# Optimization experiments

Hardware: AMD Instinct MI355X
Metric: run time of the kernel (lower is better)

The kernel has to match this reference:

```python
import jax, jax.numpy as jnp
import numpy as np

N, D, E, P, L = 50000, 128, 800000, 9, 3
EPS = 1e-5  # torch nn.LayerNorm default eps


def _layernorm(x, g, b):
    m = jnp.mean(x, axis=-1, keepdims=True)
    v = jnp.mean((x - m) ** 2, axis=-1, keepdims=True)
    return (x - m) * jax.lax.rsqrt(v + EPS) * g + b


def _pol_transform(x, M, onehot):
    # x: (N,d), M: (P,d,d), onehot: (N,P). Equivalent to bmm(x[n] @ M[pol[n]])
    # without materializing the (N,d,d) gathered map tensor.
    return jnp.einsum('nd,np,pdk->nk', x, onehot, M)


def setup_inputs() -> dict:
    key = jax.random.key(0)
    ks = jax.random.split(key, 12)
    s = 1.0 / np.sqrt(D)  # xavier-ish scale
    f32 = jnp.float32
    return {
        'x': jax.random.normal(ks[0], (N, D), f32),
        'edge_index': jax.random.randint(ks[1], (2, E), 0, N),
        'ring_polarities': jax.random.randint(ks[2], (N,), 0, P),
        'Wr': jax.random.normal(ks[3], (L, D, D), f32) * s,          # restriction weights
        'S': jax.random.normal(ks[4], (L, P, D, D), f32) * s,        # send_maps
        'dS': jax.random.normal(ks[5], (L, P, D, D), f32) * 0.01,    # delta_send
        'R': jax.random.normal(ks[6], (L, P, D, D), f32) * s,        # receive_maps
        'dR': jax.random.normal(ks[7], (L, P, D, D), f32) * 0.01,    # delta_receive
        'res_scale': jnp.full((L,), 0.92, f32),
        'W1': jax.random.normal(ks[8], (L, D, D), f32) * s,          # update Linear 1
        'b1': jnp.zeros((L, D), f32),
        'ln_g': jnp.ones((L, D), f32),                               # update LayerNorm
        'ln_b': jnp.zeros((L, D), f32),
        'W2': jax.random.normal(ks[9], (L, D, D), f32) * s,          # update Linear 2
        'b2': jnp.zeros((L, D), f32),
        'norm_g': jnp.ones((L, D), f32),                             # output LayerNorm
        'norm_b': jnp.zeros((L, D), f32),
    }


def reference(x, edge_index, ring_polarities, Wr, S, dS, R, dR, res_scale,
              W1, b1, ln_g, ln_b, W2, b2, norm_g, norm_b):
    src, tgt = edge_index[0], edge_index[1]
    pol = ring_polarities % P
    onehot = jax.nn.one_hot(pol, P, dtype=x.dtype)  # (N,P)
    # deg is accumulated over row(=src) in the original code, then used to
    # normalize the scatter over col(=tgt) -- preserved faithfully.
    deg = jax.ops.segment_sum(jnp.ones((E,), x.dtype), src, num_segments=N)
    deg_norm = (1.0 / jnp.clip(deg, 1.0))[:, None]  # (N,1)

    residual = x
    for l in range(L):
        # send transform: map depends only on src-node polarity, so apply
        # per-node then gather (algebraically identical to per-edge bmm).
        xt = _pol_transform(x, S[l] + dS[l], onehot)          # (N,D)
        msg = xt[src] @ Wr[l].T                               # (E,D) restriction per edge
        agg = jax.ops.segment_sum(msg, tgt, num_segments=N)   # index_add scatter
        # receive transform depends only on tgt polarity; linear, so it
        # commutes with the sum over incoming edges.
        out = _pol_transform(agg, R[l] + dR[l], onehot) * deg_norm
        # update MLP (dropout inactive in eval)
        h = jax.nn.relu(_layernorm(out @ W1[l].T + b1[l], ln_g[l], ln_b[l]))
        out = h @ W2[l].T + b2[l]
        out = res_scale[l] * out + x                           # in==out residual
        x = _layernorm(out, norm_g[l], norm_b[l])
    return x + residual  # stack-level residual (res_proj is None, dims match)
```

## Files before the change

kernel.cpp:

```cpp
#include <hip/hip_runtime.h>
#include <hip/hip_bf16.h>

constexpr int N_ = 50000;
constexpr int D_ = 128;
constexpr int E_ = 800000;
constexpr int P_ = 9;
constexpr int L_ = 3;
constexpr float EPS_ = 1e-5f;

constexpr int TM = 128;
constexpr int CHUNK = 4096;
constexpr int NBK = (E_ + CHUNK - 1) / CHUNK;
constexpr int NBUK = 196;
constexpr int HHALF = 256 * NBK;
constexpr int HTOT = 2 * HHALF;
constexpr int NSB = HTOT / 1024;
constexpr int MAT = L_ * P_;

typedef short bf16x8 __attribute__((ext_vector_type(8)));
typedef float f32x4 __attribute__((ext_vector_type(4)));

#define GLD16(gp, lp)                                                        \
    __builtin_amdgcn_global_load_lds(                                        \
        (const __attribute__((address_space(1))) unsigned int*)(gp),         \
        (__attribute__((address_space(3))) unsigned int*)(lp), 16, 0, 0)

__device__ inline unsigned short f2bf(float f) {
    __hip_bfloat16 h = __float2bfloat16(f);
    return *reinterpret_cast<unsigned short*>(&h);
}
__device__ inline float bflo(unsigned u) { return __uint_as_float(u << 16); }
__device__ inline float bfhi(unsigned u) { return __uint_as_float(u & 0xffff0000u); }
__device__ inline float bf2f(unsigned short h) {
    return __uint_as_float((unsigned)h << 16);
}
__device__ inline unsigned pack2bf(float a, float b) {
    return (unsigned)f2bf(a) | ((unsigned)f2bf(b) << 16);
}


__global__ __launch_bounds__(256) void setup_nk(const int* __restrict__ ring,
                                                int* __restrict__ pol,
                                                int* __restrict__ bcnt,
                                                const int* __restrict__ ei,
                                                int* __restrict__ histG) {
    __shared__ int h[P_];
    __shared__ int hT[256], hS[256];
    int blk = blockIdx.x, tid = threadIdx.x;
    if (tid < P_) h[tid] = 0;
    hT[tid] = 0;
    hS[tid] = 0;
    __syncthreads();
    int n = blk * 256 + tid;
    if (n < N_) {
        int p = ring[n] % P_;
        pol[n] = p;
        atomicAdd(&h[p], 1);
    }
    int base = blk * CHUNK;
#pragma unroll
    for (int i = 0; i < CHUNK / 256; ++i) {
        int e = base + tid + i * 256;
        if (e < E_) {
            atomicAdd(&hS[ei[e] >> 8], 1);
            atomicAdd(&hT[ei[E_ + e] >> 8], 1);
        }
    }
    __syncthreads();
    if (tid < P_ && h[tid] > 0) atomicAdd(&bcnt[tid], h[tid]);
    histG[tid * NBK + blk] = hT[tid];
    histG[HHALF + tid * NBK + blk] = hS[tid];
}


__global__ __launch_bounds__(1024) void scanH1(int* __restrict__ a,
                                               int* __restrict__ blkSum) {
    __shared__ int wsum[16];
    int tid = threadIdx.x, lane = tid & 63, wid = tid >> 6;
    int idx = blockIdx.x * 1024 + tid;
    int v = a[idx];
    int inc = v;
#pragma unroll
    for (int o = 1; o < 64; o <<= 1) {
        int t = __shfl_up(inc, o, 64);
        if (lane >= o) inc += t;
    }
    if (lane == 63) wsum[wid] = inc;
    __syncthreads();
    if (tid < 16) {
        int s = wsum[tid];
#pragma unroll
        for (int o = 1; o < 16; o <<= 1) {
            int t = __shfl_up(s, o, 64);
            if (tid >= o) s += t;
        }
        wsum[tid] = s;
    }
    __syncthreads();
    int wexcl = (wid == 0) ? 0 : wsum[wid - 1];
    a[idx] = wexcl + inc - v;
    if (tid == 1023) blkSum[blockIdx.x] = wsum[15];
}

__global__ void scanH2(const int* __restrict__ blkSum, int* __restrict__ blkOff,
                       int* __restrict__ offT, const int* __restrict__ bcnt,
                       int* __restrict__ boff, int* __restrict__ tileOff) {
    if (threadIdx.x != 0) return;
    int run = 0;
    for (int i = 0; i < NSB; ++i) {
        blkOff[i] = run;
        run += blkSum[i];
    }
    offT[N_] = E_;
    boff[0] = 0;
    tileOff[0] = 0;
    for (int p = 0; p < P_; ++p) {
        boff[p + 1] = boff[p] + bcnt[p];
        tileOff[p + 1] = tileOff[p] + (bcnt[p] + TM - 1) / TM;
    }
}

__global__ __launch_bounds__(1024) void scanH3(int* __restrict__ a,
                                               const int* __restrict__ blkOff) {
    int idx = blockIdx.x * 1024 + threadIdx.x;
    a[idx] += blkOff[blockIdx.x];
}


__global__ __launch_bounds__(256) void scatterTS(const int* __restrict__ ei,
                                                 const int* __restrict__ histG,
                                                 unsigned* __restrict__ bufT,
                                                 unsigned char* __restrict__ bufS8) {
    __shared__ int ldsT[256], ldsS[256];
    int blk = blockIdx.x, tid = threadIdx.x;
    ldsT[tid] = histG[tid * NBK + blk];
    ldsS[tid] = histG[HHALF + tid * NBK + blk] - E_;
    __syncthreads();
    int base = blk * CHUNK;
#pragma unroll
    for (int i = 0; i < CHUNK / 256; ++i) {
        int e = base + tid + i * 256;
        if (e < E_) {
            int s = ei[e], t = ei[E_ + e];
            int pT = atomicAdd(&ldsT[t >> 8], 1);
            bufT[pT] = ((unsigned)t << 16) | (unsigned)s;
            int pS = atomicAdd(&ldsS[s >> 8], 1);
            bufS8[pS] = (unsigned char)(s & 255);
        }
    }
}


__global__ __launch_bounds__(256) void finalize3(
    const unsigned* __restrict__ bufT, const unsigned char* __restrict__ bufS8,
    const int* __restrict__ histG, int* __restrict__ offT,
    unsigned short* __restrict__ eSrc, float* __restrict__ dnorm,
    const int* __restrict__ pol, const int* __restrict__ boff,
    int* __restrict__ bcur, int* __restrict__ blist) {
    __shared__ int s0[256];
    __shared__ int s1[256];
    int bb = blockIdx.x, tid = threadIdx.x;

    if (bb < NBUK) {
        int b = bb;
        int start = histG[b * NBK];
        int end = histG[(b + 1) * NBK];
        s0[tid] = 0;
        __syncthreads();
        for (int i = start + tid; i < end; i += 256)
            atomicAdd(&s0[(bufT[i] >> 16) & 255], 1);
        __syncthreads();
        if (tid < 64) {
            int b0 = 4 * tid;
            int v0 = s0[b0], v1 = s0[b0 + 1], v2 = s0[b0 + 2], v3 = s0[b0 + 3];
            int lsum = v0 + v1 + v2 + v3;
            int inc = lsum;
#pragma unroll
            for (int o = 1; o < 64; o <<= 1) {
                int t = __shfl_up(inc, o, 64);
                if (tid >= o) inc += t;
            }
            int excl = inc - lsum;
            s1[b0] = excl;
            s1[b0 + 1] = excl + v0;
            s1[b0 + 2] = excl + v0 + v1;
            s1[b0 + 3] = excl + v0 + v1 + v2;
        }
        __syncthreads();
        int node = (b << 8) + tid;
        if (node < N_) offT[node] = start + s1[tid];
        __syncthreads();
        for (int i = start + tid; i < end; i += 256) {
            unsigned pk = bufT[i];
            int pos = start + atomicAdd(&s1[(pk >> 16) & 255], 1);
            eSrc[pos] = (unsigned short)(pk & 0xFFFF);
        }
    } else if (bb < 2 * NBUK) {
        int b = bb - NBUK;
        int start = histG[HHALF + b * NBK] - E_;
        int end = histG[HHALF + (b + 1) * NBK] - E_;
        s0[tid] = 0;
        __syncthreads();
        for (int i = start + tid; i < end; i += 256) atomicAdd(&s0[bufS8[i]], 1);
        __syncthreads();
        int node = (b << 8) + tid;
        if (node < N_) {
            int dg = s0[tid];
            dnorm[node] = 1.f / (float)(dg > 1 ? dg : 1);
        }
    } else {
        int b = bb - 2 * NBUK;
        if (tid < P_) s0[tid] = 0;
        __syncthreads();
        int n = b * 256 + tid;
        int p = 0, loc = 0;
        bool act = (n < N_);
        if (act) {
            p = pol[n];
            loc = atomicAdd(&s0[p], 1);
        }
        __syncthreads();
        if (tid < P_ && s0[tid] > 0) s1[tid] = atomicAdd(&bcur[tid], s0[tid]);
        __syncthreads();
        if (act) blist[boff[p] + s1[p] + loc] = n;
    }
}


constexpr int GCONV = N_ * D_ / 4 / 256;
constexpr int GS = L_ * P_ * D_ * D_ / 256;
constexpr int GW2 = L_ * D_ * D_ / 256;
constexpr int GSPL = (MAT + 6) * 16384 / 256;
constexpr int GPREP = GCONV + 1 + GS + GW2 + GSPL;

__global__ __launch_bounds__(256) void prep_all(
    const float* __restrict__ x, unsigned short* __restrict__ xb,
    unsigned short* __restrict__ bufAb, unsigned short* __restrict__ bufBb,
    const float* __restrict__ S, const float* __restrict__ dS,
    unsigned short* __restrict__ Sb,
    const float* __restrict__ W2, unsigned short* __restrict__ W2b,
    const float* __restrict__ R, const float* __restrict__ dR,
    const float* __restrict__ W1, const float* __restrict__ Wr,
    unsigned short* __restrict__ Arh, unsigned short* __restrict__ Arl,
    unsigned short* __restrict__ W1h, unsigned short* __restrict__ W1l,
    unsigned short* __restrict__ Wrth, unsigned short* __restrict__ Wrtl) {
    int b = blockIdx.x, tid = threadIdx.x;
    if (b < GCONV) {
        int i = b * 256 + tid;
        float4 v = ((const float4*)x)[i];
        ushort4 o;
        o.x = f2bf(v.x); o.y = f2bf(v.y); o.z = f2bf(v.z); o.w = f2bf(v.w);
        ((ushort4*)xb)[i] = o;
    } else if (b < GCONV + 1) {
        if (tid < 64) {
            ((unsigned*)(xb + (size_t)N_ * D_))[tid] = 0;
            ((unsigned*)(bufAb + (size_t)N_ * D_))[tid] = 0;
            ((unsigned*)(bufBb + (size_t)N_ * D_))[tid] = 0;
        }
    } else if (b < GCONV + 1 + GS) {
        int idx = (b - GCONV - 1) * 256 + tid;
        int base = idx / (D_ * D_);
        int rem = idx % (D_ * D_);
        int c = rem / D_, d = rem % D_;
        size_t in = (size_t)base * D_ * D_ + (size_t)d * D_ + c;
        Sb[idx] = f2bf(S[in] + dS[in]);
    } else if (b < GCONV + 1 + GS + GW2) {
        int idx = (b - GCONV - 1 - GS) * 256 + tid;
        W2b[idx] = f2bf(W2[idx]);
    } else {
        constexpr int SZ1 = MAT * 16384;
        constexpr int SZ2 = SZ1 + 3 * 16384;
        int idx = (b - GCONV - 1 - GS - GW2) * 256 + tid;
        float v;
        unsigned short* oh;
        unsigned short* ol;
        int j;
        if (idx < SZ1) {
            v = R[idx] + dR[idx];
            oh = Arh; ol = Arl; j = idx;
        } else if (idx < SZ2) {
            j = idx - SZ1;
            v = W1[j];
            oh = W1h; ol = W1l;
        } else {
            j = idx - SZ2;
            int l = j >> 14, rem = j & 16383;
            int d = rem >> 7, i = rem & 127;
            v = Wr[(l << 14) + i * 128 + d];
            oh = Wrth; ol = Wrtl;
        }
        unsigned short h = f2bf(v);
        oh[j] = h;
        ol[j] = f2bf(v - bf2f(h));
    }
}


template <bool APM, bool BPM, bool OUT_SPLIT>
__global__ __launch_bounds__(256) void small_mfma(
    const unsigned short* __restrict__ Ah, const unsigned short* __restrict__ Al,
    const unsigned short* __restrict__ Bh, const unsigned short* __restrict__ Bl,
    unsigned short* __restrict__ Oh, unsigned short* __restrict__ Ol) {
    __shared__ unsigned short stg[(OUT_SPLIT ? 2 : 1) * 64 * 136];
    int tid = threadIdx.x, b = blockIdx.x;
    int mat = b >> 1, rb = b & 1;
    int l = mat / P_;
    size_t aoff = (size_t)(APM ? mat : l) * 16384 + (size_t)rb * 8192;
    size_t boff = (size_t)(BPM ? mat : l) * 16384;
    const unsigned short* ahp = Ah + aoff;
    const unsigned short* alp = Al + aoff;
    const unsigned short* bhp = Bh + boff;
    const unsigned short* blp = Bl + boff;

    int lane = tid & 63, wave = tid >> 6;
    int n = lane & 15, q = lane >> 4;
    int wr = wave * 16;

    f32x4 acc[8];
#pragma unroll
    for (int t = 0; t < 8; ++t) acc[t] = (f32x4){0.f, 0.f, 0.f, 0.f};

    int arow = (wr + n) * 128;
#pragma unroll
    for (int kc = 0; kc < 4; ++kc) {
        int ko = kc * 32 + q * 8;
        bf16x8 avh = *(const bf16x8*)(ahp + arow + ko);
        bf16x8 avl = *(const bf16x8*)(alp + arow + ko);
#pragma unroll
        for (int t = 0; t < 8; ++t) {
            int brow = (t * 16 + n) * 128;
            bf16x8 bvh = *(const bf16x8*)(bhp + brow + ko);
            bf16x8 bvl = *(const bf16x8*)(blp + brow + ko);
            acc[t] = __builtin_amdgcn_mfma_f32_16x16x32_bf16(avh, bvh, acc[t], 0, 0, 0);
            acc[t] = __builtin_amdgcn_mfma_f32_16x16x32_bf16(avh, bvl, acc[t], 0, 0, 0);
            acc[t] = __builtin_amdgcn_mfma_f32_16x16x32_bf16(avl, bvh, acc[t], 0, 0, 0);
        }
    }
#pragma unroll
    for (int t = 0; t < 8; ++t)
#pragma unroll
        for (int r = 0; r < 4; ++r) {
            int row = wr + q * 4 + r;
            float v = acc[t][r];
            unsigned short h = f2bf(v);
            stg[row * 136 + t * 16 + n] = h;
            if constexpr (OUT_SPLIT)
                stg[64 * 136 + row * 136 + t * 16 + n] = f2bf(v - bf2f(h));
        }
    __syncthreads();
    size_t obase = (size_t)mat * 16384 + (size_t)rb * 8192;
#pragma unroll
    for (int i = 0; i < 4; ++i) {
        int c = tid + i * 256;
        int r = c >> 4, off = c & 15;
        *(uint4*)(Oh + obase + r * 128 + off * 8) =
            *(const uint4*)(stg + r * 136 + off * 8);
        if constexpr (OUT_SPLIT)
            *(uint4*)(Ol + obase + r * 128 + off * 8) =
                *(const uint4*)(stg + 64 * 136 + r * 136 + off * 8);
    }
}


__device__ inline void accum_row(float* acc, uint4 r) {
    acc[0] += bflo(r.x); acc[1] += bfhi(r.x);
    acc[2] += bflo(r.y); acc[3] += bfhi(r.y);
    acc[4] += bflo(r.z); acc[5] += bfhi(r.z);
    acc[6] += bflo(r.w); acc[7] += bfhi(r.w);
}

__global__ __launch_bounds__(256) void aggregate_bf(const unsigned short* __restrict__ xt,
                                                    const int* __restrict__ offT,
                                                    const unsigned short* __restrict__ eSrc,
                                                    unsigned short* __restrict__ agg) {
    int nd = blockIdx.x * 4 + (threadIdx.x >> 6);
    if (nd >= N_) return;
    int l = threadIdx.x & 63;
    int g = l >> 4, c16 = l & 15;
    int beg = offT[nd], end = offT[nd + 1];

    float acc[8];
#pragma unroll
    for (int k = 0; k < 8; ++k) acc[k] = 0.f;

    for (int base = beg; base < end; base += 64) {
        int cnt = min(64, end - base);
        int idxv = (l < cnt) ? (int)eSrc[base + l] : 0;
        int steps = (cnt + 3) >> 2;
        int j = 0;
        for (; j + 3 < steps; j += 4) {
            int e0 = 4 * j + g, e1 = e0 + 4, e2 = e0 + 8, e3 = e0 + 12;
            int i0 = __shfl(idxv, e0, 64);
            int i1 = __shfl(idxv, e1, 64);
            int i2 = __shfl(idxv, e2, 64);
            int i3 = __shfl(idxv, e3, 64);
            int r0 = (e0 < cnt) ? i0 : N_;
            int r1 = (e1 < cnt) ? i1 : N_;
            int r2 = (e2 < cnt) ? i2 : N_;
            int r3 = (e3 < cnt) ? i3 : N_;
            uint4 v0 = ((const uint4*)(xt + (size_t)r0 * D_))[c16];
            uint4 v1 = ((const uint4*)(xt + (size_t)r1 * D_))[c16];
            uint4 v2 = ((const uint4*)(xt + (size_t)r2 * D_))[c16];
            uint4 v3 = ((const uint4*)(xt + (size_t)r3 * D_))[c16];
            accum_row(acc, v0);
            accum_row(acc, v1);
            accum_row(acc, v2);
            accum_row(acc, v3);
        }
        for (; j < steps; ++j) {
            int e0 = 4 * j + g;
            int i0 = __shfl(idxv, e0, 64);
            int r0 = (e0 < cnt) ? i0 : N_;
            uint4 v0 = ((const uint4*)(xt + (size_t)r0 * D_))[c16];
            accum_row(acc, v0);
        }
    }
#pragma unroll
    for (int k = 0; k < 8; ++k) {
        acc[k] += __shfl_xor(acc[k], 16, 64);
        acc[k] += __shfl_xor(acc[k], 32, 64);
    }
    if (g == 0) {
        uint4 o;
        o.x = (unsigned)f2bf(acc[0]) | ((unsigned)f2bf(acc[1]) << 16);
        o.y = (unsigned)f2bf(acc[2]) | ((unsigned)f2bf(acc[3]) << 16);
        o.z = (unsigned)f2bf(acc[4]) | ((unsigned)f2bf(acc[5]) << 16);
        o.w = (unsigned)f2bf(acc[6]) | ((unsigned)f2bf(acc[7]) << 16);
        ((uint4*)(agg + (size_t)nd * D_))[c16] = o;
    }
}


__device__ inline void stage_B_async(const unsigned short* __restrict__ B,
                                     unsigned short* sB, int wave, int lane) {
    int rsub = lane >> 4, cl = lane & 15;
#pragma unroll
    for (int j = 0; j < 4; ++j) {
        int seg = wave * 4 + j;
        int row = seg * 4 + rsub;
        GLD16(B + row * 128 + ((cl ^ (row & 15)) << 3), sB + seg * 512);
    }
}

#define XCH_FRAG(dst, Pl, Ph, kc)                                            \
    {                                                                        \
        unsigned a0 = __shfl(Pl[2 * (kc)], s0, 64);                          \
        unsigned b0 = __shfl(Pl[2 * (kc) + 1], s0, 64);                      \
        unsigned a1 = __shfl(Ph[2 * (kc)], s0, 64);                          \
        unsigned b1 = __shfl(Ph[2 * (kc) + 1], s0, 64);                      \
        unsigned a2 = __shfl(Pl[2 * (kc)], s1, 64);                          \
        unsigned b2 = __shfl(Pl[2 * (kc) + 1], s1, 64);                      \
        unsigned a3 = __shfl(Ph[2 * (kc)], s1, 64);                          \
        unsigned b3 = __shfl(Ph[2 * (kc) + 1], s1, 64);                      \
        union { unsigned u[4]; bf16x8 v; } fu;                               \
        fu.u[0] = hi ? b0 : a0;                                              \
        fu.u[1] = hi ? b1 : a1;                                              \
        fu.u[2] = hi ? b2 : a2;                                              \
        fu.u[3] = hi ? b3 : a3;                                              \
        dst = fu.v;                                                          \
    }


__global__ __launch_bounds__(512, 4) void gemm_xt0(
    const unsigned short* __restrict__ A, const unsigned short* __restrict__ Bw,
    unsigned short* __restrict__ OutB, const int* __restrict__ blist,
    const int* __restrict__ boff, const int* __restrict__ tileOff) {
    __shared__ unsigned short sB[128 * 128];
    int tid = threadIdx.x, b = blockIdx.x;
    if (b >= tileOff[P_]) return;
    int pp = 0;
    while (pp < P_ - 1 && b >= tileOff[pp + 1]) ++pp;
    int tb = b - tileOff[pp];
    int cnt = boff[pp + 1] - boff[pp];
    int nrows = min(TM, cnt - tb * TM);
    int rowbase = boff[pp] + tb * TM;

    int lane = tid & 63, wave = tid >> 6;
    int n = lane & 15, q = lane >> 4;
    int rr = wave * 16 + n;
    int rw = (rr < nrows) ? blist[rowbase + rr] : -1;
    size_t grow = (rw >= 0) ? (size_t)rw : (size_t)N_;

    stage_B_async(Bw + (size_t)pp * (D_ * D_), sB, wave, lane);
    bf16x8 bg[4];
#pragma unroll
    for (int kc = 0; kc < 4; ++kc)
        bg[kc] = *(const bf16x8*)(A + grow * 128 + kc * 32 + q * 8);
    __syncthreads();

    f32x4 acc[8];
#pragma unroll
    for (int t = 0; t < 8; ++t) acc[t] = (f32x4){0.f, 0.f, 0.f, 0.f};
#pragma unroll
    for (int kc = 0; kc < 4; ++kc) {
#pragma unroll
        for (int t = 0; t < 8; ++t) {
            int cs = ((((kc << 2) + q) ^ n) << 3);
            bf16x8 af = *(const bf16x8*)(sB + (t * 16 + n) * 128 + cs);
            acc[t] = __builtin_amdgcn_mfma_f32_16x16x32_bf16(af, bg[kc], acc[t], 0, 0, 0);
        }
    }
    if (rw >= 0) {
#pragma unroll
        for (int t = 0; t < 8; ++t) {
            uint2 o;
            o.x = pack2bf(acc[t][0], acc[t][1]);
            o.y = pack2bf(acc[t][2], acc[t][3]);
            *(uint2*)(OutB + (size_t)rw * 128 + t * 16 + q * 4) = o;
        }
    }
}


template <bool LAST, bool FIRST>
__global__ __launch_bounds__(512, 4) void fused_layer(
    const unsigned short* __restrict__ agg, const unsigned short* __restrict__ DmAll,
    const unsigned short* __restrict__ W2b, const unsigned short* __restrict__ SnAll,
    const int* __restrict__ blist, const int* __restrict__ boff,
    const int* __restrict__ tileOff, const float* __restrict__ dnorm,
    const float* __restrict__ b1v, const float* __restrict__ g1v,
    const float* __restrict__ e1v, const float* __restrict__ b2v,
    const float* __restrict__ g2v, const float* __restrict__ e2v,
    const float* __restrict__ rs_ptr, const float* __restrict__ x0n,
    const unsigned short* __restrict__ xpIn, unsigned short* __restrict__ xpOut,
    float* __restrict__ OutF, unsigned short* __restrict__ OutXt) {
    __shared__ unsigned short sB[128 * 128];

    int tid = threadIdx.x, b = blockIdx.x;
    if (b >= tileOff[P_]) return;
    int pp = 0;
    while (pp < P_ - 1 && b >= tileOff[pp + 1]) ++pp;
    int tb = b - tileOff[pp];
    int cnt = boff[pp + 1] - boff[pp];
    int nrows = min(TM, cnt - tb * TM);
    int rowbase = boff[pp] + tb * TM;

    int lane = tid & 63, wave = tid >> 6;
    int n = lane & 15, q = lane >> 4;
    int rr = wave * 16 + n;
    int rw = (rr < nrows) ? blist[rowbase + rr] : -1;
    size_t grow = (rw >= 0) ? (size_t)rw : (size_t)N_;
    int s0 = n + ((q & 1) << 5), s1 = s0 + 16;
    bool hi = q >= 2;

    stage_B_async(DmAll + (size_t)pp * (D_ * D_), sB, wave, lane);
    bf16x8 bg[4];
#pragma unroll
    for (int kc = 0; kc < 4; ++kc)
        bg[kc] = *(const bf16x8*)(agg + grow * 128 + kc * 32 + q * 8);
    float dn = (rw >= 0) ? dnorm[rw] : 1.f;
    __syncthreads();

    f32x4 acc[8];
#pragma unroll
    for (int t = 0; t < 8; ++t) acc[t] = (f32x4){0.f, 0.f, 0.f, 0.f};
#pragma unroll
    for (int kc = 0; kc < 4; ++kc) {
#pragma unroll
        for (int t = 0; t < 8; ++t) {
            int cs = ((((kc << 2) + q) ^ n) << 3);
            bf16x8 af = *(const bf16x8*)(sB + (t * 16 + n) * 128 + cs);
            acc[t] = __builtin_amdgcn_mfma_f32_16x16x32_bf16(af, bg[kc], acc[t], 0, 0, 0);
        }
    }

    unsigned Pl[8], Ph[8];
    {
        float rs1 = 0.f, rs2 = 0.f;
#pragma unroll
        for (int t = 0; t < 8; ++t) {
            float4 bb = *(const float4*)(b1v + t * 16 + q * 4);
#pragma unroll
            for (int r = 0; r < 4; ++r) {
                float v = dn * acc[t][r] + (&bb.x)[r];
                acc[t][r] = v;
                rs1 += v;
                rs2 += v * v;
            }
        }
        rs1 += __shfl_xor(rs1, 16, 64);
        rs1 += __shfl_xor(rs1, 32, 64);
        rs2 += __shfl_xor(rs2, 16, 64);
        rs2 += __shfl_xor(rs2, 32, 64);
        float mm = rs1 * (1.f / 128.f);
        float rv = rsqrtf(rs2 * (1.f / 128.f) - mm * mm + EPS_);
#pragma unroll
        for (int t = 0; t < 8; ++t) {
            float4 gg = *(const float4*)(g1v + t * 16 + q * 4);
            float4 ee = *(const float4*)(e1v + t * 16 + q * 4);
            float h0 = fmaxf((acc[t][0] - mm) * rv * gg.x + ee.x, 0.f);
            float h1 = fmaxf((acc[t][1] - mm) * rv * gg.y + ee.y, 0.f);
            float h2 = fmaxf((acc[t][2] - mm) * rv * gg.z + ee.z, 0.f);
            float h3 = fmaxf((acc[t][3] - mm) * rv * gg.w + ee.w, 0.f);
            Pl[t] = pack2bf(h0, h1);
            Ph[t] = pack2bf(h2, h3);
        }
    }

    __syncthreads();
    stage_B_async(W2b, sB, wave, lane);
    bf16x8 h2[4];
#pragma unroll
    for (int kc = 0; kc < 4; ++kc) XCH_FRAG(h2[kc], Pl, Ph, kc)
    __syncthreads();

#pragma unroll
    for (int t = 0; t < 8; ++t) acc[t] = (f32x4){0.f, 0.f, 0.f, 0.f};
#pragma unroll
    for (int kc = 0; kc < 4; ++kc) {
#pragma unroll
        for (int t = 0; t < 8; ++t) {
            int cs = ((((kc << 2) + q) ^ n) << 3);
            bf16x8 af = *(const bf16x8*)(sB + (t * 16 + n) * 128 + cs);
            acc[t] = __builtin_amdgcn_mfma_f32_16x16x32_bf16(af, h2[kc], acc[t], 0, 0, 0);
        }
    }

    float rsc = rs_ptr[0];
    {
        float xr4[8][4];
        if constexpr (FIRST) {
#pragma unroll
            for (int t = 0; t < 8; ++t) {
                if (rw >= 0) {
                    float4 v = *(const float4*)(x0n + (size_t)rw * 128 + t * 16 + q * 4);
                    xr4[t][0] = v.x; xr4[t][1] = v.y; xr4[t][2] = v.z; xr4[t][3] = v.w;
                } else {
                    xr4[t][0] = xr4[t][1] = xr4[t][2] = xr4[t][3] = 0.f;
                }
            }
        } else {
#pragma unroll
            for (int t = 0; t < 8; ++t) {
                if (rw >= 0) {
                    uint2 u = *(const uint2*)(xpIn + (size_t)rw * 128 + t * 16 + q * 4);
                    xr4[t][0] = bflo(u.x); xr4[t][1] = bfhi(u.x);
                    xr4[t][2] = bflo(u.y); xr4[t][3] = bfhi(u.y);
                } else {
                    xr4[t][0] = xr4[t][1] = xr4[t][2] = xr4[t][3] = 0.f;
                }
            }
        }
        float rs1 = 0.f, rs2 = 0.f;
#pragma unroll
        for (int t = 0; t < 8; ++t) {
            float4 bb = *(const float4*)(b2v + t * 16 + q * 4);
#pragma unroll
            for (int r = 0; r < 4; ++r) {
                float v = rsc * (acc[t][r] + (&bb.x)[r]) + xr4[t][r];
                acc[t][r] = v;
                rs1 += v;
                rs2 += v * v;
            }
        }
        rs1 += __shfl_xor(rs1, 16, 64);
        rs1 += __shfl_xor(rs1, 32, 64);
        rs2 += __shfl_xor(rs2, 16, 64);
        rs2 += __shfl_xor(rs2, 32, 64);
        float mm = rs1 * (1.f / 128.f);
        float rv = rsqrtf(rs2 * (1.f / 128.f) - mm * mm + EPS_);
        if constexpr (LAST) {
#pragma unroll
            for (int t = 0; t < 8; ++t) {
                float4 gg = *(const float4*)(g2v + t * 16 + q * 4);
                float4 ee = *(const float4*)(e2v + t * 16 + q * 4);
                if (rw >= 0) {
                    float4 xa = *(const float4*)(x0n + (size_t)rw * 128 + t * 16 + q * 4);
                    float4 o;
                    o.x = (acc[t][0] - mm) * rv * gg.x + ee.x + xa.x;
                    o.y = (acc[t][1] - mm) * rv * gg.y + ee.y + xa.y;
                    o.z = (acc[t][2] - mm) * rv * gg.z + ee.z + xa.z;
                    o.w = (acc[t][3] - mm) * rv * gg.w + ee.w + xa.w;
                    *(float4*)(OutF + (size_t)rw * 128 + t * 16 + q * 4) = o;
                }
            }
        } else {
#pragma unroll
            for (int t = 0; t < 8; ++t) {
                float4 gg = *(const float4*)(g2v + t * 16 + q * 4);
                float4 ee = *(const float4*)(e2v + t * 16 + q * 4);
                float o0 = (acc[t][0] - mm) * rv * gg.x + ee.x;
                float o1 = (acc[t][1] - mm) * rv * gg.y + ee.y;
                float o2 = (acc[t][2] - mm) * rv * gg.z + ee.z;
                float o3 = (acc[t][3] - mm) * rv * gg.w + ee.w;
                Pl[t] = pack2bf(o0, o1);
                Ph[t] = pack2bf(o2, o3);
            }
        }
    }

    if constexpr (!LAST) {
        __syncthreads();
        stage_B_async(SnAll + (size_t)pp * (D_ * D_), sB, wave, lane);
        bf16x8 x2[4];
#pragma unroll
        for (int kc = 0; kc < 4; ++kc) XCH_FRAG(x2[kc], Pl, Ph, kc)
        __syncthreads();

#pragma unroll
        for (int t = 0; t < 8; ++t) acc[t] = (f32x4){0.f, 0.f, 0.f, 0.f};
#pragma unroll
        for (int kc = 0; kc < 4; ++kc) {
#pragma unroll
            for (int t = 0; t < 8; ++t) {
                int cs = ((((kc << 2) + q) ^ n) << 3);
                bf16x8 af = *(const bf16x8*)(sB + (t * 16 + n) * 128 + cs);
                acc[t] = __builtin_amdgcn_mfma_f32_16x16x32_bf16(af, x2[kc], acc[t], 0, 0, 0);
            }
        }
        if (rw >= 0) {
#pragma unroll
            for (int t = 0; t < 8; ++t) {
                uint2 o;
                o.x = pack2bf(acc[t][0], acc[t][1]);
                o.y = pack2bf(acc[t][2], acc[t][3]);
                *(uint2*)(OutXt + (size_t)rw * 128 + t * 16 + q * 4) = o;
            }
#pragma unroll
            for (int t = 0; t < 8; ++t) {
                uint2 h;
                h.x = Pl[t];
                h.y = Ph[t];
                *(uint2*)(xpOut + (size_t)rw * 128 + t * 16 + q * 4) = h;
            }
        }
    }
}


extern "C" void kernel_launch(void* const* d_in, const int* in_sizes, int n_in,
                              void* d_out, int out_size, void* d_ws, size_t ws_size,
                              hipStream_t stream) {
    const float* x0 = (const float*)d_in[0];
    const int* ei = (const int*)d_in[1];
    const int* ring = (const int*)d_in[2];
    const float* Wr = (const float*)d_in[3];
    const float* S = (const float*)d_in[4];
    const float* dS = (const float*)d_in[5];
    const float* R = (const float*)d_in[6];
    const float* dR = (const float*)d_in[7];
    const float* rsc = (const float*)d_in[8];
    const float* W1 = (const float*)d_in[9];
    const float* b1 = (const float*)d_in[10];
    const float* lng = (const float*)d_in[11];
    const float* lnb = (const float*)d_in[12];
    const float* W2 = (const float*)d_in[13];
    const float* b2 = (const float*)d_in[14];
    const float* ng = (const float*)d_in[15];
    const float* nb = (const float*)d_in[16];
    float* out = (float*)d_out;

    char* w = (char*)d_ws;
    auto alloc = [&](size_t bytes) {
        char* p = w;
        w += (bytes + 15) & ~(size_t)15;
        return p;
    };
    unsigned short* xb = (unsigned short*)alloc((size_t)(N_ + 1) * D_ * 2);
    unsigned short* bufAb = (unsigned short*)alloc((size_t)(N_ + 1) * D_ * 2);
    unsigned short* bufBb = (unsigned short*)alloc((size_t)(N_ + 1) * D_ * 2);
    unsigned short* xpb = (unsigned short*)alloc((size_t)(N_ + 1) * D_ * 2);
    unsigned short* Sb = (unsigned short*)alloc((size_t)L_ * P_ * D_ * D_ * 2);
    unsigned short* Dmb = (unsigned short*)alloc((size_t)L_ * P_ * D_ * D_ * 2);
    unsigned short* W2b = (unsigned short*)alloc((size_t)L_ * D_ * D_ * 2);
    unsigned short* Arh = (unsigned short*)alloc((size_t)MAT * 16384 * 2);
    unsigned short* Arl = (unsigned short*)alloc((size_t)MAT * 16384 * 2);
    unsigned short* W1h = (unsigned short*)alloc((size_t)3 * 16384 * 2);
    unsigned short* W1l = (unsigned short*)alloc((size_t)3 * 16384 * 2);
    unsigned short* Wrth = (unsigned short*)alloc((size_t)3 * 16384 * 2);
    unsigned short* Wrtl = (unsigned short*)alloc((size_t)3 * 16384 * 2);
    unsigned short* T1th = (unsigned short*)alloc((size_t)MAT * 16384 * 2);
    unsigned short* T1tl = (unsigned short*)alloc((size_t)MAT * 16384 * 2);
    float* dnorm = (float*)alloc((size_t)N_ * 4);
    int* histG = (int*)alloc((size_t)HTOT * 4);
    unsigned* bufT = (unsigned*)alloc((size_t)E_ * 4);
    unsigned char* bufS8 = (unsigned char*)alloc((size_t)E_);
    unsigned short* eSrc = (unsigned short*)alloc((size_t)E_ * 2);
    int* offT = (int*)alloc((size_t)(N_ + 1) * 4);
    int* pol = (int*)alloc((size_t)N_ * 4);
    int* boff = (int*)alloc((size_t)(P_ + 1) * 4);
    int* tileOff = (int*)alloc((size_t)(P_ + 1) * 4);
    int* blist = (int*)alloc((size_t)N_ * 4);
    int* blkSum = (int*)alloc((size_t)NSB * 4);
    int* blkOff = (int*)alloc((size_t)NSB * 4);
    int* bcnt = (int*)alloc((size_t)2 * P_ * 4);
    int* bcur = bcnt + P_;

    hipMemsetAsync(bcnt, 0, (size_t)2 * P_ * 4, stream);

    const int BTILES = N_ / TM + P_;

    setup_nk<<<NBK, 256, 0, stream>>>(ring, pol, bcnt, ei, histG);
    scanH1<<<NSB, 1024, 0, stream>>>(histG, blkSum);
    scanH2<<<1, 64, 0, stream>>>(blkSum, blkOff, offT, bcnt, boff, tileOff);
    scanH3<<<NSB, 1024, 0, stream>>>(histG, blkOff);
    scatterTS<<<NBK, 256, 0, stream>>>(ei, histG, bufT, bufS8);
    finalize3<<<3 * NBUK, 256, 0, stream>>>(bufT, bufS8, histG, offT, eSrc, dnorm,
                                            pol, boff, bcur, blist);
    prep_all<<<GPREP, 256, 0, stream>>>(x0, xb, bufAb, bufBb, S, dS, Sb, W2, W2b,
                                        R, dR, W1, Wr, Arh, Arl, W1h, W1l, Wrth, Wrtl);
    small_mfma<false, true, true><<<2 * MAT, 256, 0, stream>>>(
        W1h, W1l, Arh, Arl, T1th, T1tl);
    small_mfma<true, false, false><<<2 * MAT, 256, 0, stream>>>(
        T1th, T1tl, Wrth, Wrtl, Dmb, nullptr);

    gemm_xt0<<<BTILES, 512, 0, stream>>>(xb, Sb, bufAb, blist, boff, tileOff);

    for (int l = 0; l < L_; ++l) {
        const size_t lPDD = (size_t)l * P_ * D_ * D_;
        const size_t lDD = (size_t)l * D_ * D_;
        const size_t lD = (size_t)l * D_;
        aggregate_bf<<<N_ / 4, 256, 0, stream>>>(bufAb, offT, eSrc, bufBb);
        if (l == 0) {
            fused_layer<false, true><<<BTILES, 512, 0, stream>>>(
                bufBb, Dmb + lPDD, W2b + lDD, Sb + lPDD + (size_t)P_ * D_ * D_,
                blist, boff, tileOff, dnorm,
                b1 + lD, lng + lD, lnb + lD, b2 + lD, ng + lD, nb + lD,
                rsc + l, x0, nullptr, xpb, nullptr, bufAb);
        } else if (l < L_ - 1) {
            fused_layer<false, false><<<BTILES, 512, 0, stream>>>(
                bufBb, Dmb + lPDD, W2b + lDD, Sb + lPDD + (size_t)P_ * D_ * D_,
                blist, boff, tileOff, dnorm,
                b1 + lD, lng + lD, lnb + lD, b2 + lD, ng + lD, nb + lD,
                rsc + l, nullptr, xpb, xpb, nullptr, bufAb);
        } else {
            fused_layer<true, false><<<BTILES, 512, 0, stream>>>(
                bufBb, Dmb + lPDD, W2b + lDD, nullptr,
                blist, boff, tileOff, dnorm,
                b1 + lD, lng + lD, lnb + lD, b2 + lD, ng + lD, nb + lD,
                rsc + l, x0, xpb, nullptr, out, nullptr);
        }
    }
}
```

Measured before the change: 360.1 us.

## Fold scan fixup kernels into scatter and merge finalize with prep

Removes the scanH2 and scanH3 launches. Each consumer block now recomputes the block-offset prefix of the histogram from blkSum in shared memory and adds it on the fly. The finalize3 work is merged into the prep_all launch as extra blocks, so the independent conversion work overlaps with CSR finalization and two fewer kernel launches and dependency gaps occur. The cost is a redundant serial prefix over NSB entries in every block.

```diff
diff --git a/kernel.cpp b/kernel.cpp
--- a/kernel.cpp
+++ b/kernel.cpp
@@ -102,39 +102,30 @@
     if (tid == 1023) blkSum[blockIdx.x] = wsum[15];
 }
 
-__global__ void scanH2(const int* __restrict__ blkSum, int* __restrict__ blkOff,
-                       int* __restrict__ offT, const int* __restrict__ bcnt,
-                       int* __restrict__ boff, int* __restrict__ tileOff) {
-    if (threadIdx.x != 0) return;
-    int run = 0;
-    for (int i = 0; i < NSB; ++i) {
-        blkOff[i] = run;
-        run += blkSum[i];
-    }
-    offT[N_] = E_;
-    boff[0] = 0;
-    tileOff[0] = 0;
-    for (int p = 0; p < P_; ++p) {
-        boff[p + 1] = boff[p] + bcnt[p];
-        tileOff[p + 1] = tileOff[p] + (bcnt[p] + TM - 1) / TM;
-    }
-}
-
-__global__ __launch_bounds__(1024) void scanH3(int* __restrict__ a,
-                                               const int* __restrict__ blkOff) {
-    int idx = blockIdx.x * 1024 + threadIdx.x;
-    a[idx] += blkOff[blockIdx.x];
-}
-
 
 __global__ __launch_bounds__(256) void scatterTS(const int* __restrict__ ei,
                                                  const int* __restrict__ histG,
+                                                 const int* __restrict__ blkSum,
                                                  unsigned* __restrict__ bufT,
                                                  unsigned char* __restrict__ bufS8) {
     __shared__ int ldsT[256], ldsS[256];
+    __shared__ int bOff[NSB];
     int blk = blockIdx.x, tid = threadIdx.x;
-    ldsT[tid] = histG[tid * NBK + blk];
-    ldsS[tid] = histG[HHALF + tid * NBK + blk] - E_;
+    if (tid < NSB) bOff[tid] = blkSum[tid];
+    __syncthreads();
+    if (tid == 0) {
+        int run = 0;
+        for (int i = 0; i < NSB; ++i) {
+            int t = bOff[i];
+            bOff[i] = run;
+            run += t;
+        }
+    }
+    __syncthreads();
+    int i1 = tid * NBK + blk;
+    int i2 = HHALF + i1;
+    ldsT[tid] = histG[i1] + bOff[i1 >> 10];
+    ldsS[tid] = histG[i2] + bOff[i2 >> 10] - E_;
     __syncthreads();
     int base = blk * CHUNK;
 #pragma unroll
@@ -151,89 +142,14 @@
 }
 
 
-__global__ __launch_bounds__(256) void finalize3(
-    const unsigned* __restrict__ bufT, const unsigned char* __restrict__ bufS8,
-    const int* __restrict__ histG, int* __restrict__ offT,
-    unsigned short* __restrict__ eSrc, float* __restrict__ dnorm,
-    const int* __restrict__ pol, const int* __restrict__ boff,
-    int* __restrict__ bcur, int* __restrict__ blist) {
-    __shared__ int s0[256];
-    __shared__ int s1[256];
-    int bb = blockIdx.x, tid = threadIdx.x;
-
-    if (bb < NBUK) {
-        int b = bb;
-        int start = histG[b * NBK];
-        int end = histG[(b + 1) * NBK];
-        s0[tid] = 0;
-        __syncthreads();
-        for (int i = start + tid; i < end; i += 256)
-            atomicAdd(&s0[(bufT[i] >> 16) & 255], 1);
-        __syncthreads();
-        if (tid < 64) {
-            int b0 = 4 * tid;
-            int v0 = s0[b0], v1 = s0[b0 + 1], v2 = s0[b0 + 2], v3 = s0[b0 + 3];
-            int lsum = v0 + v1 + v2 + v3;
-            int inc = lsum;
-#pragma unroll
-            for (int o = 1; o < 64; o <<= 1) {
-                int t = __shfl_up(inc, o, 64);
-                if (tid >= o) inc += t;
-            }
-            int excl = inc - lsum;
-            s1[b0] = excl;
-            s1[b0 + 1] = excl + v0;
-            s1[b0 + 2] = excl + v0 + v1;
-            s1[b0 + 3] = excl + v0 + v1 + v2;
-        }
-        __syncthreads();
-        int node = (b << 8) + tid;
-        if (node < N_) offT[node] = start + s1[tid];
-        __syncthreads();
-        for (int i = start + tid; i < end; i += 256) {
-            unsigned pk = bufT[i];
-            int pos = start + atomicAdd(&s1[(pk >> 16) & 255], 1);
-            eSrc[pos] = (unsigned short)(pk & 0xFFFF);
-        }
-    } else if (bb < 2 * NBUK) {
-        int b = bb - NBUK;
-        int start = histG[HHALF + b * NBK] - E_;
-        int end = histG[HHALF + (b + 1) * NBK] - E_;
-        s0[tid] = 0;
-        __syncthreads();
-        for (int i = start + tid; i < end; i += 256) atomicAdd(&s0[bufS8[i]], 1);
-        __syncthreads();
-        int node = (b << 8) + tid;
-        if (node < N_) {
-            int dg = s0[tid];
-            dnorm[node] = 1.f / (float)(dg > 1 ? dg : 1);
-        }
-    } else {
-        int b = bb - 2 * NBUK;
-        if (tid < P_) s0[tid] = 0;
-        __syncthreads();
-        int n = b * 256 + tid;
-        int p = 0, loc = 0;
-        bool act = (n < N_);
-        if (act) {
-            p = pol[n];
-            loc = atomicAdd(&s0[p], 1);
-        }
-        __syncthreads();
-        if (tid < P_ && s0[tid] > 0) s1[tid] = atomicAdd(&bcur[tid], s0[tid]);
-        __syncthreads();
-        if (act) blist[boff[p] + s1[p] + loc] = n;
-    }
-}
-
-
 constexpr int GCONV = N_ * D_ / 4 / 256;
 constexpr int GS = L_ * P_ * D_ * D_ / 256;
 constexpr int GW2 = L_ * D_ * D_ / 256;
 constexpr int GSPL = (MAT + 6) * 16384 / 256;
 constexpr int GPREP = GCONV + 1 + GS + GW2 + GSPL;
-
-__global__ __launch_bounds__(256) void prep_all(
+constexpr int GFIN = GPREP + 3 * NBUK;
+
+__global__ __launch_bounds__(256) void finprep(
     const float* __restrict__ x, unsigned short* __restrict__ xb,
     unsigned short* __restrict__ bufAb, unsigned short* __restrict__ bufBb,
     const float* __restrict__ S, const float* __restrict__ dS,
@@ -243,8 +159,19 @@
     const float* __restrict__ W1, const float* __restrict__ Wr,
     unsigned short* __restrict__ Arh, unsigned short* __restrict__ Arl,
     unsigned short* __restrict__ W1h, unsigned short* __restrict__ W1l,
-    unsigned short* __restrict__ Wrth, unsigned short* __restrict__ Wrtl) {
+    unsigned short* __restrict__ Wrth, unsigned short* __restrict__ Wrtl,
+    const unsigned* __restrict__ bufT, const unsigned char* __restrict__ bufS8,
+    const int* __restrict__ histG, const int* __restrict__ blkSum,
+    int* __restrict__ offT, unsigned short* __restrict__ eSrc,
+    float* __restrict__ dnorm, const int* __restrict__ pol,
+    const int* __restrict__ bcnt, int* __restrict__ bcur,
+    int* __restrict__ blist, int* __restrict__ boffG, int* __restrict__ tileOffG) {
+    __shared__ int s0[256];
+    __shared__ int s1[256];
+    __shared__ int bOffs[NSB];
+    __shared__ int boffL[P_ + 1];
     int b = blockIdx.x, tid = threadIdx.x;
+
     if (b < GCONV) {
         int i = b * 256 + tid;
         float4 v = ((const float4*)x)[i];
@@ -267,7 +194,7 @@
     } else if (b < GCONV + 1 + GS + GW2) {
         int idx = (b - GCONV - 1 - GS) * 256 + tid;
         W2b[idx] = f2bf(W2[idx]);
-    } else {
+    } else if (b < GPREP) {
         constexpr int SZ1 = MAT * 16384;
         constexpr int SZ2 = SZ1 + 3 * 16384;
         int idx = (b - GCONV - 1 - GS - GW2) * 256 + tid;
@@ -292,6 +219,112 @@
         unsigned short h = f2bf(v);
         oh[j] = h;
         ol[j] = f2bf(v - bf2f(h));
+    } else {
+        int bb = b - GPREP;
+        if (bb < NBUK) {
+            int bk = bb;
+            if (tid < NSB) bOffs[tid] = blkSum[tid];
+            s0[tid] = 0;
+            __syncthreads();
+            if (tid == 0) {
+                int run = 0;
+                for (int i = 0; i < NSB; ++i) {
+                    int t = bOffs[i];
+                    bOffs[i] = run;
+                    run += t;
+                }
+            }
+            __syncthreads();
+            int i0 = bk * NBK, i1 = (bk + 1) * NBK;
+            int start = histG[i0] + bOffs[i0 >> 10];
+            int end = histG[i1] + bOffs[i1 >> 10];
+            for (int i = start + tid; i < end; i += 256)
+                atomicAdd(&s0[(bufT[i] >> 16) & 255], 1);
+            __syncthreads();
+            if (tid < 64) {
+                int b0 = 4 * tid;
+                int v0 = s0[b0], v1 = s0[b0 + 1], v2 = s0[b0 + 2], v3 = s0[b0 + 3];
+                int lsum = v0 + v1 + v2 + v3;
+                int inc = lsum;
+#pragma unroll
+                for (int o = 1; o < 64; o <<= 1) {
+                    int t = __shfl_up(inc, o, 64);
+                    if (tid >= o) inc += t;
+                }
+                int excl = inc - lsum;
+                s1[b0] = excl;
+                s1[b0 + 1] = excl + v0;
+                s1[b0 + 2] = excl + v0 + v1;
+                s1[b0 + 3] = excl + v0 + v1 + v2;
+            }
+            __syncthreads();
+            int node = (bk << 8) + tid;
+            if (node < N_) offT[node] = start + s1[tid];
+            __syncthreads();
+            for (int i = start + tid; i < end; i += 256) {
+                unsigned pk = bufT[i];
+                int pos = start + atomicAdd(&s1[(pk >> 16) & 255], 1);
+                eSrc[pos] = (unsigned short)(pk & 0xFFFF);
+            }
+        } else if (bb < 2 * NBUK) {
+            int bk = bb - NBUK;
+            if (tid < NSB) bOffs[tid] = blkSum[tid];
+            s0[tid] = 0;
+            __syncthreads();
+            if (tid == 0) {
+                int run = 0;
+                for (int i = 0; i < NSB; ++i) {
+                    int t = bOffs[i];
+                    bOffs[i] = run;
+                    run += t;
+                }
+            }
+            __syncthreads();
+            int i0 = HHALF + bk * NBK, i1 = HHALF + (bk + 1) * NBK;
+            int start = histG[i0] + bOffs[i0 >> 10] - E_;
+            int end = histG[i1] + bOffs[i1 >> 10] - E_;
+            for (int i = start + tid; i < end; i += 256) atomicAdd(&s0[bufS8[i]], 1);
+            __syncthreads();
+            int node = (bk << 8) + tid;
+            if (node < N_) {
+                int dg = s0[tid];
+                dnorm[node] = 1.f / (float)(dg > 1 ? dg : 1);
+            }
+        } else {
+            int bk = bb - 2 * NBUK;
+            if (tid == 0) {
+                int run = 0;
+                for (int p = 0; p < P_; ++p) {
+                    boffL[p] = run;
+                    run += bcnt[p];
+                }
+                boffL[P_] = run;
+            }
+            if (tid < P_) s0[tid] = 0;
+            __syncthreads();
+            if (bk == 0 && tid == 0) {
+                offT[N_] = E_;
+                int runT = 0;
+                for (int p = 0; p < P_; ++p) {
+                    boffG[p] = boffL[p];
+                    tileOffG[p] = runT;
+                    runT += (bcnt[p] + TM - 1) / TM;
+                }
+                boffG[P_] = boffL[P_];
+                tileOffG[P_] = runT;
+            }
+            int n = bk * 256 + tid;
+            int p = 0, loc = 0;
+            bool act = (n < N_);
+            if (act) {
+                p = pol[n];
+                loc = atomicAdd(&s0[p], 1);
+            }
+            __syncthreads();
+            if (tid < P_ && s0[tid] > 0) s1[tid] = atomicAdd(&bcur[tid], s0[tid]);
+            __syncthreads();
+            if (act) blist[boffL[p] + s1[p] + loc] = n;
+        }
     }
 }
 
@@ -782,7 +815,6 @@
     int* tileOff = (int*)alloc((size_t)(P_ + 1) * 4);
     int* blist = (int*)alloc((size_t)N_ * 4);
     int* blkSum = (int*)alloc((size_t)NSB * 4);
-    int* blkOff = (int*)alloc((size_t)NSB * 4);
     int* bcnt = (int*)alloc((size_t)2 * P_ * 4);
     int* bcur = bcnt + P_;
 
@@ -792,13 +824,12 @@
 
     setup_nk<<<NBK, 256, 0, stream>>>(ring, pol, bcnt, ei, histG);
     scanH1<<<NSB, 1024, 0, stream>>>(histG, blkSum);
-    scanH2<<<1, 64, 0, stream>>>(blkSum, blkOff, offT, bcnt, boff, tileOff);
-    scanH3<<<NSB, 1024, 0, stream>>>(histG, blkOff);
-    scatterTS<<<NBK, 256, 0, stream>>>(ei, histG, bufT, bufS8);
-    finalize3<<<3 * NBUK, 256, 0, stream>>>(bufT, bufS8, histG, offT, eSrc, dnorm,
-                                            pol, boff, bcur, blist);
-    prep_all<<<GPREP, 256, 0, stream>>>(x0, xb, bufAb, bufBb, S, dS, Sb, W2, W2b,
-                                        R, dR, W1, Wr, Arh, Arl, W1h, W1l, Wrth, Wrtl);
+    scatterTS<<<NBK, 256, 0, stream>>>(ei, histG, blkSum, bufT, bufS8);
+    finprep<<<GFIN, 256, 0, stream>>>(
+        x0, xb, bufAb, bufBb, S, dS, Sb, W2, W2b, R, dR, W1, Wr,
+        Arh, Arl, W1h, W1l, Wrth, Wrtl,
+        bufT, bufS8, histG, blkSum, offT, eSrc, dnorm, pol, bcnt, bcur,
+        blist, boff, tileOff);
     small_mfma<false, true, true><<<2 * MAT, 256, 0, stream>>>(
         W1h, W1l, Arh, Arl, T1th, T1tl);
     small_mfma<true, false, false><<<2 * MAT, 256, 0, stream>>>(
```

Result: no change. 357.7 us (-0.7%).
